# Kernel optimization log

Hardware: AMD Instinct MI355X
Metric: run time of the kernel (lower is better)

## Reference

```python
import jax, jax.numpy as jnp
import numpy as np

B, N, F_IN, F_OUT = 8, 2048, 256, 128
ALPHA = 0.2
NEG_BIG = -9000000000000000.0


def setup_inputs() -> dict:
    key = jax.random.key(0)
    k1, k2, k3, k4 = jax.random.split(key, 4)
    X = jax.random.normal(k1, (B, N, F_IN), dtype=jnp.float32)
    # sparse-ish binary adjacency with self loops (faithful: module only needs 0/1 mask)
    A = (jax.random.uniform(k2, (B, N, N)) < 0.05).astype(jnp.float32)
    eye = jnp.eye(N, dtype=jnp.float32)[None]
    A = jnp.maximum(A, eye)
    # xavier_uniform-style init
    limW = float(np.sqrt(6.0 / (F_IN + F_OUT)))
    W = jax.random.uniform(k3, (F_IN, F_OUT), minval=-limW, maxval=limW, dtype=jnp.float32)
    lima = float(np.sqrt(6.0 / (2 * F_OUT + 1)))
    a = jax.random.uniform(k4, (2 * F_OUT, 1), minval=-lima, maxval=lima, dtype=jnp.float32)
    return {"X": X, "A": A, "W": W, "a": a}


def reference(X, A, W, a):
    # Wh: [B, N, F_OUT]
    Wh = jnp.einsum('bni,io->bno', X, W)
    # split a into source/dest halves: e_ij = leaky_relu(a1.Wh_i + a2.Wh_j)
    # (algebraically identical to cat([Wh_i, Wh_j]) @ a, avoids BxNxNx2F tensor)
    a1 = a[:F_OUT, 0]   # [F_OUT]
    a2 = a[F_OUT:, 0]   # [F_OUT]
    s1 = Wh @ a1        # [B, N]
    s2 = Wh @ a2        # [B, N]
    e = jax.nn.leaky_relu(s1[:, :, None] + s2[:, None, :], negative_slope=ALPHA)  # [B,N,N]
    e = e + NEG_BIG * (1.0 - A)
    attention = jax.nn.softmax(e, axis=-1)
    h_prime = jnp.einsum('bmn,bno->bmo', attention, Wh)
    return h_prime
```

## Files before the change

### kernel.cpp

```cpp
#include <hip/hip_runtime.h>
#include <math.h>

#define B_DIM 8
#define N_DIM 2048
#define F_IN 256
#define F_OUT 128
#define ALPHA 0.2f
#define KPAD 136
#define NSPLIT 4
#define TPB 4
#define PS ((size_t)B_DIM * N_DIM * F_OUT)

typedef __attribute__((ext_vector_type(8))) short short8;
typedef __attribute__((ext_vector_type(4))) float floatx4;

static __device__ __forceinline__ unsigned short f2bf(float f) {
    unsigned u = __float_as_uint(f);
    u += 0x7fff + ((u >> 16) & 1);
    return (unsigned short)(u >> 16);
}
static __device__ __forceinline__ float bf2f(unsigned short s) {
    return __uint_as_float((unsigned)s << 16);
}
static __device__ __forceinline__ unsigned fmap(float f) {
    int b = __float_as_int(f);
    return (unsigned)(b ^ ((b >> 31) | 0x80000000));
}
static __device__ __forceinline__ float funmap(unsigned u) {
    return __uint_as_float((u & 0x80000000u) ? (int)(u ^ 0x80000000u) : ~(int)u);
}

__global__ __launch_bounds__(256) void gemm_xw(const float* __restrict__ X,
                                               const float* __restrict__ W,
                                               const float* __restrict__ avec,
                                               unsigned short* __restrict__ WhT,
                                               float* __restrict__ s1,
                                               float* __restrict__ s2,
                                               unsigned* __restrict__ s2max_u) {
    __shared__ unsigned short Wt[F_OUT][KPAD];
    const int t = threadIdx.x;
    const int lane = t & 63, wave = t >> 6;
    const int m = lane & 15, q = lane >> 4;
    const int row0 = blockIdx.x * 64 + wave * 16;

    floatx4 acc[8];
#pragma unroll
    for (int nt = 0; nt < 8; nt++) acc[nt] = (floatx4){0.f, 0.f, 0.f, 0.f};

    const int n0 = (t & 31) * 4;
    const int kb = t >> 5;

    for (int half = 0; half < 2; half++) {
        const float* Wp = W + (size_t)(half * 128 + kb) * F_OUT + n0;
#pragma unroll
        for (int i = 0; i < 16; i++) {
            float4 w = *(const float4*)(Wp + (size_t)i * 8 * F_OUT);
            int kk = kb + i * 8;
            Wt[n0 + 0][kk] = f2bf(w.x);
            Wt[n0 + 1][kk] = f2bf(w.y);
            Wt[n0 + 2][kk] = f2bf(w.z);
            Wt[n0 + 3][kk] = f2bf(w.w);
        }
        __syncthreads();

        const float* xrow = X + (size_t)(row0 + m) * F_IN + half * 128 + q * 8;
        float4 xr[8];
#pragma unroll
        for (int kt = 0; kt < 4; kt++) {
            xr[2 * kt] = *(const float4*)(xrow + kt * 32);
            xr[2 * kt + 1] = *(const float4*)(xrow + kt * 32 + 4);
        }
#pragma unroll
        for (int kt = 0; kt < 4; kt++) {
            union { unsigned short u[8]; short8 v; } af;
            float tmp[8] = {xr[2 * kt].x, xr[2 * kt].y, xr[2 * kt].z, xr[2 * kt].w,
                            xr[2 * kt + 1].x, xr[2 * kt + 1].y, xr[2 * kt + 1].z, xr[2 * kt + 1].w};
#pragma unroll
            for (int j = 0; j < 8; j++) af.u[j] = f2bf(tmp[j]);
#pragma unroll
            for (int nt = 0; nt < 8; nt++) {
                short8 bv = *(const short8*)&Wt[nt * 16 + m][kt * 32 + q * 8];
                acc[nt] = __builtin_amdgcn_mfma_f32_16x16x32_bf16(af.v, bv, acc[nt], 0, 0, 0);
            }
        }
        __syncthreads();
    }

    const int b = row0 >> 11;
    unsigned short* WTb = WhT + (size_t)b * F_OUT * N_DIM;
#pragma unroll
    for (int nt = 0; nt < 8; nt++) {
#pragma unroll
        for (int r = 0; r < 4; r++) {
            int nloc = (row0 & 2047) + q * 4 + r;
            WTb[(size_t)(nt * 16 + m) * N_DIM + nloc] = f2bf(acc[nt][r]);
        }
    }
    float a1v[8], a2v[8];
#pragma unroll
    for (int nt = 0; nt < 8; nt++) {
        a1v[nt] = avec[nt * 16 + m];
        a2v[nt] = avec[F_OUT + nt * 16 + m];
    }
    float wmax = -1e30f;
#pragma unroll
    for (int r = 0; r < 4; r++) {
        float v1 = 0.f, v2 = 0.f;
#pragma unroll
        for (int nt = 0; nt < 8; nt++) {
            v1 = fmaf(acc[nt][r], a1v[nt], v1);
            v2 = fmaf(acc[nt][r], a2v[nt], v2);
        }
#pragma unroll
        for (int mk = 8; mk >= 1; mk >>= 1) {
            v1 += __shfl_xor(v1, mk, 64);
            v2 += __shfl_xor(v2, mk, 64);
        }
        if (m == 0) {
            int row = row0 + q * 4 + r;
            s1[row] = v1;
            s2[row] = v2;
        }
        wmax = fmaxf(wmax, v2);
    }
    wmax = fmaxf(wmax, __shfl_xor(wmax, 16, 64));
    wmax = fmaxf(wmax, __shfl_xor(wmax, 32, 64));
    if (lane == 0) atomicMax(&s2max_u[b], fmap(wmax));
}

__global__ __launch_bounds__(256) void attn_mm(const float* __restrict__ A,
                                               const unsigned short* __restrict__ WhT,
                                               const float* __restrict__ s1,
                                               const float* __restrict__ s2,
                                               const unsigned* __restrict__ s2max_u,
                                               float* __restrict__ pacc,
                                               float* __restrict__ plsum) {
    __shared__ unsigned short Bs[2048 * 8];

    const int t = threadIdx.x;
    const int lane = t & 63, wave = t >> 6;
    const int m = lane & 15, q = lane >> 4;
    const int ns = blockIdx.x >> 8;
    const int rg = blockIdx.x & 255;
    const int row0 = rg * 64;
    const int b = row0 >> 11;
    const int nbase = ns * 512;

    const unsigned short* WTb = WhT + (size_t)b * F_OUT * N_DIM;
    const int myrow = row0 + wave * 16 + m;
    const float s1m = s1[myrow];
    const float s2mx = funmap(s2max_u[b]);
    const float xs = s1m + s2mx;
    const float shift = fmaxf(xs, ALPHA * xs);
    const float* Arow = A + (size_t)myrow * N_DIM;
    const float* s2b = s2 + (size_t)b * N_DIM;

    const int c_s0 = t >> 6;

    floatx4 acc[8];
#pragma unroll
    for (int nt = 0; nt < 8; nt++) acc[nt] = (floatx4){0.f, 0.f, 0.f, 0.f};
    float lsum = 0.f;

    for (int tl = 0; tl < TPB; tl++) {
        const int noff = nbase + tl * 128;

        float4 areg[8], zreg[8];
#pragma unroll
        for (int c = 0; c < 4; c++) {
            areg[2 * c] = *(const float4*)(Arow + noff + c * 32 + q * 8);
            areg[2 * c + 1] = *(const float4*)(Arow + noff + c * 32 + q * 8 + 4);
            zreg[2 * c] = *(const float4*)(s2b + noff + c * 32 + q * 8);
            zreg[2 * c + 1] = *(const float4*)(s2b + noff + c * 32 + q * 8 + 4);
        }
        uint4 sreg[8];
#pragma unroll
        for (int i = 0; i < 8; i++) {
            int iw = i * 4 + c_s0;
            int cs = iw & 3, nts = iw >> 2;
            sreg[i] = *(const uint4*)(WTb + (size_t)(nts * 16 + m) * N_DIM + noff + cs * 32 + q * 8);
        }

        short8 pf[4];
#pragma unroll
        for (int c = 0; c < 4; c++) {
            float aa[8] = {areg[2 * c].x, areg[2 * c].y, areg[2 * c].z, areg[2 * c].w,
                           areg[2 * c + 1].x, areg[2 * c + 1].y, areg[2 * c + 1].z, areg[2 * c + 1].w};
            float zz[8] = {zreg[2 * c].x, zreg[2 * c].y, zreg[2 * c].z, zreg[2 * c].w,
                           zreg[2 * c + 1].x, zreg[2 * c + 1].y, zreg[2 * c + 1].z, zreg[2 * c + 1].w};
            union { unsigned short u[8]; short8 v; } pu;
#pragma unroll
            for (int j = 0; j < 8; j++) {
                float x = s1m + zz[j];
                float e = fmaxf(x, ALPHA * x);
                float p = aa[j] * __expf(e - shift);
                unsigned short pb = f2bf(p);
                pu.u[j] = pb;
                lsum += bf2f(pb);
            }
            pf[c] = pu.v;
        }

#pragma unroll
        for (int i = 0; i < 8; i++)
            *(uint4*)&Bs[(size_t)(i * 256 + t) * 8] = sreg[i];
        __syncthreads();

#pragma unroll
        for (int c = 0; c < 4; c++)
#pragma unroll
            for (int nt = 0; nt < 8; nt++) {
                short8 bv = *(const short8*)&Bs[(size_t)((nt * 4 + c) * 64 + lane) * 8];
                acc[nt] = __builtin_amdgcn_mfma_f32_16x16x32_bf16(pf[c], bv, acc[nt], 0, 0, 0);
            }
        __syncthreads();
    }

    lsum += __shfl_xor(lsum, 16, 64);
    lsum += __shfl_xor(lsum, 32, 64);
    if (q == 0) plsum[(size_t)ns * (B_DIM * N_DIM) + row0 + wave * 16 + m] = lsum;

    float* pa = pacc + (size_t)ns * PS;
#pragma unroll
    for (int r = 0; r < 4; r++) {
        float* prow = pa + (size_t)(row0 + wave * 16 + q * 4 + r) * F_OUT + m;
#pragma unroll
        for (int nt = 0; nt < 8; nt++) prow[nt * 16] = acc[nt][r];
    }
}

__global__ __launch_bounds__(256) void epi(const float* __restrict__ pacc,
                                           const float* __restrict__ plsum,
                                           float* __restrict__ out) {
    const int t = threadIdx.x;
    const int row = blockIdx.x * 8 + (t >> 5);
    const int c0 = (t & 31) * 4;
    float l = 0.f;
#pragma unroll
    for (int ns = 0; ns < NSPLIT; ns++) l += plsum[(size_t)ns * (B_DIM * N_DIM) + row];
    float4 v = make_float4(0.f, 0.f, 0.f, 0.f);
#pragma unroll
    for (int ns = 0; ns < NSPLIT; ns++) {
        float4 p = *(const float4*)(pacc + (size_t)ns * PS + (size_t)row * F_OUT + c0);
        v.x += p.x; v.y += p.y; v.z += p.z; v.w += p.w;
    }
    const float inv = 1.f / l;
    v.x *= inv; v.y *= inv; v.z *= inv; v.w *= inv;
    *(float4*)(out + (size_t)row * F_OUT + c0) = v;
}

extern "C" void kernel_launch(void* const* d_in, const int* in_sizes, int n_in,
                              void* d_out, int out_size, void* d_ws, size_t ws_size,
                              hipStream_t stream) {
    const float* X = (const float*)d_in[0];
    const float* A = (const float*)d_in[1];
    const float* W = (const float*)d_in[2];
    const float* avec = (const float*)d_in[3];
    float* out = (float*)d_out;

    char* ws = (char*)d_ws;
    unsigned short* WhT = (unsigned short*)ws;            ws += PS * 2;
    float* s1 = (float*)ws;                               ws += B_DIM * N_DIM * 4;
    float* s2 = (float*)ws;                               ws += B_DIM * N_DIM * 4;
    unsigned* s2max_u = (unsigned*)ws;                    ws += 256;
    float* pacc = (float*)ws;                             ws += PS * NSPLIT * 4;
    float* plsum = (float*)ws;

    hipMemsetAsync(s2max_u, 0, B_DIM * sizeof(unsigned), stream);
    gemm_xw<<<B_DIM * N_DIM / 64, 256, 0, stream>>>(X, W, avec, WhT, s1, s2, s2max_u);
    attn_mm<<<256 * NSPLIT, 256, 0, stream>>>(A, WhT, s1, s2, s2max_u, pacc, plsum);
    epi<<<B_DIM * N_DIM / 8, 256, 0, stream>>>(pacc, plsum, out);
}
```

Measured before the change: 258.9 us.

## Transpose gemm MFMA operands, stage s2 in LDS, reorder loads, add occupancy hint

In gemm_xw the MFMA operands are swapped so each lane holds four consecutive output features for one row. That simplifies the s1/s2 dot products: float4 loads of the attention vector and fewer shuffle reductions. In attn_mm the per-block s2 slice is staged once in shared memory instead of being re-read from global memory each tile. The WhT loads and their LDS stores are moved ahead of the exp computation, and launch_bounds(256,2) is added to encourage two blocks per CU. The row sum now accumulates the fp32 probability rather than its bf16-rounded value, a slight numeric inconsistency with the bf16 numerator.

```diff
diff --git a/kernel.cpp b/kernel.cpp
--- a/kernel.cpp
+++ b/kernel.cpp
@@ -18,9 +18,6 @@
     unsigned u = __float_as_uint(f);
     u += 0x7fff + ((u >> 16) & 1);
     return (unsigned short)(u >> 16);
-}
-static __device__ __forceinline__ float bf2f(unsigned short s) {
-    return __uint_as_float((unsigned)s << 16);
 }
 static __device__ __forceinline__ unsigned fmap(float f) {
     int b = __float_as_int(f);
@@ -45,7 +42,7 @@
 
     floatx4 acc[8];
 #pragma unroll
-    for (int nt = 0; nt < 8; nt++) acc[nt] = (floatx4){0.f, 0.f, 0.f, 0.f};
+    for (int ft = 0; ft < 8; ft++) acc[ft] = (floatx4){0.f, 0.f, 0.f, 0.f};
 
     const int n0 = (t & 31) * 4;
     const int kb = t >> 5;
@@ -72,70 +69,63 @@
         }
 #pragma unroll
         for (int kt = 0; kt < 4; kt++) {
-            union { unsigned short u[8]; short8 v; } af;
+            union { unsigned short u[8]; short8 v; } xf;
             float tmp[8] = {xr[2 * kt].x, xr[2 * kt].y, xr[2 * kt].z, xr[2 * kt].w,
                             xr[2 * kt + 1].x, xr[2 * kt + 1].y, xr[2 * kt + 1].z, xr[2 * kt + 1].w};
 #pragma unroll
-            for (int j = 0; j < 8; j++) af.u[j] = f2bf(tmp[j]);
-#pragma unroll
-            for (int nt = 0; nt < 8; nt++) {
-                short8 bv = *(const short8*)&Wt[nt * 16 + m][kt * 32 + q * 8];
-                acc[nt] = __builtin_amdgcn_mfma_f32_16x16x32_bf16(af.v, bv, acc[nt], 0, 0, 0);
+            for (int j = 0; j < 8; j++) xf.u[j] = f2bf(tmp[j]);
+#pragma unroll
+            for (int ft = 0; ft < 8; ft++) {
+                short8 wv = *(const short8*)&Wt[ft * 16 + m][kt * 32 + q * 8];
+                acc[ft] = __builtin_amdgcn_mfma_f32_16x16x32_bf16(wv, xf.v, acc[ft], 0, 0, 0);
             }
         }
         __syncthreads();
     }
 
     const int b = row0 >> 11;
+    const int nloc = (row0 & 2047) + m;
     unsigned short* WTb = WhT + (size_t)b * F_OUT * N_DIM;
 #pragma unroll
-    for (int nt = 0; nt < 8; nt++) {
+    for (int ft = 0; ft < 8; ft++) {
 #pragma unroll
         for (int r = 0; r < 4; r++) {
-            int nloc = (row0 & 2047) + q * 4 + r;
-            WTb[(size_t)(nt * 16 + m) * N_DIM + nloc] = f2bf(acc[nt][r]);
-        }
-    }
-    float a1v[8], a2v[8];
-#pragma unroll
-    for (int nt = 0; nt < 8; nt++) {
-        a1v[nt] = avec[nt * 16 + m];
-        a2v[nt] = avec[F_OUT + nt * 16 + m];
-    }
-    float wmax = -1e30f;
-#pragma unroll
-    for (int r = 0; r < 4; r++) {
-        float v1 = 0.f, v2 = 0.f;
-#pragma unroll
-        for (int nt = 0; nt < 8; nt++) {
-            v1 = fmaf(acc[nt][r], a1v[nt], v1);
-            v2 = fmaf(acc[nt][r], a2v[nt], v2);
-        }
-#pragma unroll
-        for (int mk = 8; mk >= 1; mk >>= 1) {
-            v1 += __shfl_xor(v1, mk, 64);
-            v2 += __shfl_xor(v2, mk, 64);
-        }
-        if (m == 0) {
-            int row = row0 + q * 4 + r;
-            s1[row] = v1;
-            s2[row] = v2;
-        }
-        wmax = fmaxf(wmax, v2);
-    }
-    wmax = fmaxf(wmax, __shfl_xor(wmax, 16, 64));
-    wmax = fmaxf(wmax, __shfl_xor(wmax, 32, 64));
+            int f = ft * 16 + q * 4 + r;
+            WTb[(size_t)f * N_DIM + nloc] = f2bf(acc[ft][r]);
+        }
+    }
+
+    float v1 = 0.f, v2 = 0.f;
+#pragma unroll
+    for (int ft = 0; ft < 8; ft++) {
+        float4 a1q = *(const float4*)&avec[ft * 16 + q * 4];
+        float4 a2q = *(const float4*)&avec[F_OUT + ft * 16 + q * 4];
+        v1 = fmaf(acc[ft][0], a1q.x, v1); v1 = fmaf(acc[ft][1], a1q.y, v1);
+        v1 = fmaf(acc[ft][2], a1q.z, v1); v1 = fmaf(acc[ft][3], a1q.w, v1);
+        v2 = fmaf(acc[ft][0], a2q.x, v2); v2 = fmaf(acc[ft][1], a2q.y, v2);
+        v2 = fmaf(acc[ft][2], a2q.z, v2); v2 = fmaf(acc[ft][3], a2q.w, v2);
+    }
+    v1 += __shfl_xor(v1, 16, 64); v1 += __shfl_xor(v1, 32, 64);
+    v2 += __shfl_xor(v2, 16, 64); v2 += __shfl_xor(v2, 32, 64);
+    if (lane < 16) {
+        s1[row0 + m] = v1;
+        s2[row0 + m] = v2;
+    }
+    float wmax = v2;
+#pragma unroll
+    for (int mk = 8; mk >= 1; mk >>= 1) wmax = fmaxf(wmax, __shfl_xor(wmax, mk, 64));
     if (lane == 0) atomicMax(&s2max_u[b], fmap(wmax));
 }
 
-__global__ __launch_bounds__(256) void attn_mm(const float* __restrict__ A,
-                                               const unsigned short* __restrict__ WhT,
-                                               const float* __restrict__ s1,
-                                               const float* __restrict__ s2,
-                                               const unsigned* __restrict__ s2max_u,
-                                               float* __restrict__ pacc,
-                                               float* __restrict__ plsum) {
+__global__ __launch_bounds__(256, 2) void attn_mm(const float* __restrict__ A,
+                                                  const unsigned short* __restrict__ WhT,
+                                                  const float* __restrict__ s1,
+                                                  const float* __restrict__ s2,
+                                                  const unsigned* __restrict__ s2max_u,
+                                                  float* __restrict__ pacc,
+                                                  float* __restrict__ plsum) {
     __shared__ unsigned short Bs[2048 * 8];
+    __shared__ float s2l[512];
 
     const int t = threadIdx.x;
     const int lane = t & 63, wave = t >> 6;
@@ -147,63 +137,63 @@
     const int nbase = ns * 512;
 
     const unsigned short* WTb = WhT + (size_t)b * F_OUT * N_DIM;
+    if (t < 128) *(float4*)&s2l[t * 4] = ((const float4*)(s2 + (size_t)b * N_DIM + nbase))[t];
+
     const int myrow = row0 + wave * 16 + m;
     const float s1m = s1[myrow];
     const float s2mx = funmap(s2max_u[b]);
     const float xs = s1m + s2mx;
     const float shift = fmaxf(xs, ALPHA * xs);
-    const float* Arow = A + (size_t)myrow * N_DIM;
-    const float* s2b = s2 + (size_t)b * N_DIM;
-
-    const int c_s0 = t >> 6;
+    const float* Arow = A + (size_t)myrow * N_DIM + nbase;
+
+    const int iw0 = t >> 6;
 
     floatx4 acc[8];
 #pragma unroll
     for (int nt = 0; nt < 8; nt++) acc[nt] = (floatx4){0.f, 0.f, 0.f, 0.f};
     float lsum = 0.f;
 
+    __syncthreads();
+
     for (int tl = 0; tl < TPB; tl++) {
-        const int noff = nbase + tl * 128;
-
-        float4 areg[8], zreg[8];
+        const int noff = tl * 128;
+
+        uint4 sreg[8];
+#pragma unroll
+        for (int i = 0; i < 8; i++) {
+            int iw = i * 4 + iw0;
+            int cs = iw & 3, nts = iw >> 2;
+            sreg[i] = *(const uint4*)(WTb + (size_t)(nts * 16 + m) * N_DIM + nbase + noff + cs * 32 + q * 8);
+        }
+        float4 areg[8];
 #pragma unroll
         for (int c = 0; c < 4; c++) {
             areg[2 * c] = *(const float4*)(Arow + noff + c * 32 + q * 8);
             areg[2 * c + 1] = *(const float4*)(Arow + noff + c * 32 + q * 8 + 4);
-            zreg[2 * c] = *(const float4*)(s2b + noff + c * 32 + q * 8);
-            zreg[2 * c + 1] = *(const float4*)(s2b + noff + c * 32 + q * 8 + 4);
-        }
-        uint4 sreg[8];
-#pragma unroll
-        for (int i = 0; i < 8; i++) {
-            int iw = i * 4 + c_s0;
-            int cs = iw & 3, nts = iw >> 2;
-            sreg[i] = *(const uint4*)(WTb + (size_t)(nts * 16 + m) * N_DIM + noff + cs * 32 + q * 8);
-        }
+        }
+#pragma unroll
+        for (int i = 0; i < 8; i++)
+            *(uint4*)&Bs[(size_t)(i * 256 + t) * 8] = sreg[i];
 
         short8 pf[4];
 #pragma unroll
         for (int c = 0; c < 4; c++) {
+            float4 za = *(const float4*)&s2l[noff + c * 32 + q * 8];
+            float4 zb = *(const float4*)&s2l[noff + c * 32 + q * 8 + 4];
             float aa[8] = {areg[2 * c].x, areg[2 * c].y, areg[2 * c].z, areg[2 * c].w,
                            areg[2 * c + 1].x, areg[2 * c + 1].y, areg[2 * c + 1].z, areg[2 * c + 1].w};
-            float zz[8] = {zreg[2 * c].x, zreg[2 * c].y, zreg[2 * c].z, zreg[2 * c].w,
-                           zreg[2 * c + 1].x, zreg[2 * c + 1].y, zreg[2 * c + 1].z, zreg[2 * c + 1].w};
+            float zz[8] = {za.x, za.y, za.z, za.w, zb.x, zb.y, zb.z, zb.w};
             union { unsigned short u[8]; short8 v; } pu;
 #pragma unroll
             for (int j = 0; j < 8; j++) {
                 float x = s1m + zz[j];
                 float e = fmaxf(x, ALPHA * x);
                 float p = aa[j] * __expf(e - shift);
-                unsigned short pb = f2bf(p);
-                pu.u[j] = pb;
-                lsum += bf2f(pb);
+                pu.u[j] = f2bf(p);
+                lsum += p;
             }
             pf[c] = pu.v;
         }
-
-#pragma unroll
-        for (int i = 0; i < 8; i++)
-            *(uint4*)&Bs[(size_t)(i * 256 + t) * 8] = sreg[i];
         __syncthreads();
 
 #pragma unroll
```

Measured after the change: 265.5 us. +2.5%, slower.
